# Kernel tuning notes

Hardware: AMD Instinct MI355X
Metric: run time of the kernel (lower is better)

The kernel has to match this reference:

```python
import jax, jax.numpy as jnp
import numpy as np

B, S, D_MODEL = 2, 2048, 4096
N_HEADS, N_KV, HEAD_DIM = 32, 8, 128
N_GROUPS = N_HEADS // N_KV
QKV_DIM = (N_HEADS + 2 * N_KV) * HEAD_DIM


def _rope_tables(seq_len, head_dim, base=10000.0):
    inv_freq = 1.0 / (base ** (np.arange(0, head_dim, 2, dtype=np.float32) / head_dim))
    t = np.arange(seq_len, dtype=np.float32)
    freqs = np.outer(t, inv_freq)                      # [S, D/2]
    emb = np.concatenate([freqs, freqs], axis=-1)      # [S, D]
    return jnp.asarray(np.cos(emb)), jnp.asarray(np.sin(emb))


def setup_inputs() -> dict:
    key = jax.random.key(0)
    k1, k2, k3 = jax.random.split(key, 3)
    cos, sin = _rope_tables(S, HEAD_DIM)
    return {
        "hidden_states": jax.random.normal(k1, (B, S, D_MODEL), dtype=jnp.float32),
        "cos": cos,
        "sin": sin,
        "W_qkv": jax.random.normal(k2, (D_MODEL, QKV_DIM), dtype=jnp.float32) * (D_MODEL ** -0.5),
        "W_out": jax.random.normal(k3, (D_MODEL, D_MODEL), dtype=jnp.float32) * (D_MODEL ** -0.5),
    }


def _rotate_half(x):
    x1, x2 = jnp.split(x, 2, axis=-1)
    return jnp.concatenate([-x2, x1], axis=-1)


def _apply_rope(x, cos, sin):
    # x: [b, h, s, d]; cos/sin: [s, d]
    c = cos[None, None, :, :]
    s = sin[None, None, :, :]
    return x * c + _rotate_half(x) * s


def reference(hidden_states, cos, sin, W_qkv, W_out):
    b, s, _ = hidden_states.shape
    qkv = jnp.einsum("bsm,mq->bsq", hidden_states, W_qkv)
    q_end = N_HEADS * HEAD_DIM
    kv_sz = N_KV * HEAD_DIM
    q = qkv[..., :q_end].reshape(b, s, N_HEADS, HEAD_DIM).transpose(0, 2, 1, 3)
    k = qkv[..., q_end:q_end + kv_sz].reshape(b, s, N_KV, HEAD_DIM).transpose(0, 2, 1, 3)
    v = qkv[..., q_end + kv_sz:].reshape(b, s, N_KV, HEAD_DIM).transpose(0, 2, 1, 3)

    q = _apply_rope(q, cos, sin)          # [b, H, s, d]
    k = _apply_rope(k, cos, sin)          # [b, KV, s, d] (equiv. to repeat->rope->stride slice)

    # GQA without materializing repeated KV: group query heads per KV head.
    qg = q.reshape(b, N_KV, N_GROUPS, s, HEAD_DIM)
    scale = HEAD_DIM ** -0.5
    scores = jnp.einsum("bkgqd,bkpd->bkgqp", qg, k) * scale  # [b, KV, G, s, s]
    causal = jnp.tril(jnp.ones((s, s), dtype=bool))
    scores = jnp.where(causal, scores, jnp.finfo(scores.dtype).min)
    probs = jax.nn.softmax(scores, axis=-1)
    out = jnp.einsum("bkgqp,bkpd->bkgqd", probs, v)           # [b, KV, G, s, d]
    out = out.reshape(b, N_HEADS, s, HEAD_DIM).transpose(0, 2, 1, 3).reshape(b, s, D_MODEL)
    return jnp.einsum("bsm,mn->bsn", out, W_out)
```

## Files before the change

### kernel.cpp

```cpp
#include <hip/hip_runtime.h>


typedef __bf16 bf16;
typedef bf16 bf16x8 __attribute__((ext_vector_type(8)));
typedef bf16 bf16x4 __attribute__((ext_vector_type(4)));
typedef float f32x4 __attribute__((ext_vector_type(4)));
typedef unsigned int u32;
typedef u32 u32x4 __attribute__((ext_vector_type(4)));

#define B_ 2
#define S_ 2048
#define DM 4096
#define NH 32
#define NKV 8
#define HD 128
#define QKV_DIM 6144

typedef __attribute__((address_space(3))) void lds_void;
typedef const __attribute__((address_space(1))) void glb_void;

__device__ __forceinline__ void gld_lds16(const bf16* g, bf16* l) {
  __builtin_amdgcn_global_load_lds((glb_void*)g, (lds_void*)l, 16, 0, 0);
}

__device__ __forceinline__ u32 bf16bits(float x) {
  union { bf16 h; unsigned short s; } u;
  u.h = (bf16)x;
  return (u32)u.s;
}

__global__ __launch_bounds__(256) void cast_f32_bf16(const float* __restrict__ src,
                                                     bf16* __restrict__ dst, int n) {
  int i = (blockIdx.x * 256 + threadIdx.x) * 4;
  float4 v = *(const float4*)(src + i);
  bf16x4 o;
  o[0] = (bf16)v.x; o[1] = (bf16)v.y; o[2] = (bf16)v.z; o[3] = (bf16)v.w;
  *(bf16x4*)(dst + i) = o;
}

__global__ __launch_bounds__(256) void transpose_cast_w(const float* __restrict__ W,
                                                        bf16* __restrict__ Wt,
                                                        int K, int N) {
  __shared__ float tile[64][65];
  const int n0 = blockIdx.x * 64, k0 = blockIdx.y * 64;
  const int t = threadIdx.x, j = t & 63, i0 = t >> 6;
  for (int p = 0; p < 16; ++p) {
    int i = i0 + p * 4;
    tile[i][j] = W[(size_t)(k0 + i) * N + n0 + j];
  }
  __syncthreads();
  for (int p = 0; p < 16; ++p) {
    int n = i0 + p * 4;
    Wt[(size_t)(n0 + n) * K + k0 + j] = (bf16)tile[j][n];
  }
}

__global__ __launch_bounds__(256) void transpose_v(const bf16* __restrict__ qkv,
                                                   bf16* __restrict__ v_t) {
  __shared__ bf16 tile[64][65];
  const int s0 = blockIdx.x * 64;
  const int d0 = blockIdx.y * 64;
  const int bk = blockIdx.z;
  const int b = bk >> 3, kv = bk & 7;
  const int t = threadIdx.x, j = t & 63, i0 = t >> 6;
  const bf16* src = qkv + (size_t)b * S_ * QKV_DIM + 5120 + kv * HD;
  for (int p = 0; p < 16; ++p) {
    int i = i0 + p * 4;
    tile[i][j] = src[(size_t)(s0 + i) * QKV_DIM + d0 + j];
  }
  __syncthreads();
  bf16* dst = v_t + ((size_t)bk * HD + d0) * S_ + s0;
  for (int p = 0; p < 16; ++p) {
    int dd = i0 + p * 4;
    dst[(size_t)dd * S_ + j] = tile[j][dd];
  }
}

__global__ __launch_bounds__(128) void rope_kernel(const bf16* __restrict__ qkv,
                                                   const float* __restrict__ cosT,
                                                   const float* __restrict__ sinT,
                                                   bf16* __restrict__ q_r,
                                                   bf16* __restrict__ k_r) {
  const int bs = blockIdx.x;
  const int b = bs >> 11, s = bs & 2047;
  const int d = threadIdx.x;
  const float cv = cosT[s * HD + d];
  const float sv = sinT[s * HD + d];
  const bf16* row = qkv + (size_t)bs * QKV_DIM;
  const float scale = 0.08838834764831845f;
  for (int h = 0; h < NH; ++h) {
    float x = (float)row[h * HD + d];
    float xr = (d < 64) ? -(float)row[h * HD + d + 64] : (float)row[h * HD + d - 64];
    q_r[(((size_t)(b * NH + h)) * S_ + s) * HD + d] = (bf16)((x * cv + xr * sv) * scale);
  }
  for (int kv = 0; kv < NKV; ++kv) {
    float x = (float)row[DM + kv * HD + d];
    float xr = (d < 64) ? -(float)row[DM + kv * HD + d + 64] : (float)row[DM + kv * HD + d - 64];
    k_r[(((size_t)(b * NKV + kv)) * S_ + s) * HD + d] = (bf16)(x * cv + xr * sv);
  }
}

template <bool OUT_BF16>
__global__ __launch_bounds__(256) void gemm_bt(const bf16* __restrict__ A,
                                               const bf16* __restrict__ Bt,
                                               void* __restrict__ Cout,
                                               int M, int N, int K) {
  __shared__ bf16 As[128 * 32];
  __shared__ bf16 Bs[128 * 32];
  const int m0 = blockIdx.y * 128, n0 = blockIdx.x * 128;
  const int t = threadIdx.x;
  const int lane = t & 63, w = t >> 6;
  const int wm = (w >> 1) * 64, wn = (w & 1) * 64;
  const int quad = lane >> 4, c = lane & 15;

  f32x4 acc[4][4] = {};

  const int s0i = t;
  const int r0 = s0i >> 2, c0 = (s0i & 3) * 8;
  const int s1i = 256 + t;
  const int r1 = s1i >> 2, c1 = (s1i & 3) * 8;
  const bf16* Ap0 = A + (size_t)(m0 + r0) * K + c0;
  const bf16* Ap1 = A + (size_t)(m0 + r1) * K + c1;
  const bf16* Bp0 = Bt + (size_t)(n0 + r0) * K + c0;
  const bf16* Bp1 = Bt + (size_t)(n0 + r1) * K + c1;
  bf16* Asl0 = As + (size_t)(w * 64) * 8;
  bf16* Asl1 = As + (size_t)(256 + w * 64) * 8;
  bf16* Bsl0 = Bs + (size_t)(w * 64) * 8;
  bf16* Bsl1 = Bs + (size_t)(256 + w * 64) * 8;

  for (int k0 = 0; k0 < K; k0 += 32) {
    gld_lds16(Ap0 + k0, Asl0);
    gld_lds16(Ap1 + k0, Asl1);
    gld_lds16(Bp0 + k0, Bsl0);
    gld_lds16(Bp1 + k0, Bsl1);
    __syncthreads();

    bf16x8 af[4], bfr[4];
#pragma unroll
    for (int i = 0; i < 4; ++i)
      af[i] = *(const bf16x8*)(As + (wm + i * 16 + c) * 32 + quad * 8);
#pragma unroll
    for (int j = 0; j < 4; ++j)
      bfr[j] = *(const bf16x8*)(Bs + (wn + j * 16 + c) * 32 + quad * 8);
#pragma unroll
    for (int i = 0; i < 4; ++i)
#pragma unroll
      for (int j = 0; j < 4; ++j)
        acc[i][j] = __builtin_amdgcn_mfma_f32_16x16x32_bf16(af[i], bfr[j], acc[i][j], 0, 0, 0);
    __syncthreads();
  }

#pragma unroll
  for (int i = 0; i < 4; ++i)
#pragma unroll
    for (int j = 0; j < 4; ++j) {
      const int row = m0 + wm + i * 16 + quad * 4;
      const int col = n0 + wn + j * 16 + c;
      if constexpr (OUT_BF16) {
        bf16* Cp = (bf16*)Cout;
#pragma unroll
        for (int r = 0; r < 4; ++r) Cp[(size_t)(row + r) * N + col] = (bf16)acc[i][j][r];
      } else {
        float* Cp = (float*)Cout;
#pragma unroll
        for (int r = 0; r < 4; ++r) Cp[(size_t)(row + r) * N + col] = acc[i][j][r];
      }
    }
}

#define SKS 136
#define SVS 40
__global__ __launch_bounds__(256) void attn_kernel(const bf16* __restrict__ q_r,
                                                   const bf16* __restrict__ k_r,
                                                   const bf16* __restrict__ v_t,
                                                   bf16* __restrict__ attn_out) {
  __shared__ bf16 Ks[32 * SKS];
  __shared__ bf16 Vs[128 * SVS];

  const int bh = blockIdx.x;
  const int b = bh >> 5, h = bh & 31;
  const int kv = h >> 2;
  const int q0 = blockIdx.y * 64;
  const int t = threadIdx.x, w = t >> 6, lane = t & 63;
  const int quad = lane >> 4, c = lane & 15;
  const int myq = q0 + w * 16 + c;

  const bf16* qrow = q_r + ((size_t)(b * NH + h) * S_ + myq) * HD;
  bf16x8 qf[4];
#pragma unroll
  for (int kk = 0; kk < 4; ++kk) qf[kk] = *(const bf16x8*)(qrow + quad * 8 + kk * 32);

  float m_i = -1e30f, l_i = 0.f;
  f32x4 o_acc[8];
#pragma unroll
  for (int n = 0; n < 8; ++n) o_acc[n] = (f32x4){0.f, 0.f, 0.f, 0.f};

  const bf16* kb_ptr = k_r + (size_t)(b * NKV + kv) * S_ * HD;
  const bf16* vb_ptr = v_t + (size_t)(b * NKV + kv) * HD * S_;

  const int nch = (q0 + 64) >> 5;
  const int ks_key = t >> 3, ks_doff = (t & 7) * 16;
  const int vs_d = t >> 1, vs_koff = (t & 1) * 16;
  const int src0 = c + 32 * (quad & 1);
  const int src1 = src0 + 16;
  const bool hiTile = (quad & 2) != 0;

  for (int ch = 0; ch < nch; ++ch) {
    const int kb = ch * 32;
    __syncthreads();
    {
      const bf16* kp = kb_ptr + (size_t)(kb + ks_key) * HD + ks_doff;
      bf16x8 kv0 = *(const bf16x8*)(kp);
      bf16x8 kv1 = *(const bf16x8*)(kp + 8);
      const bf16* vp = vb_ptr + (size_t)vs_d * S_ + kb + vs_koff;
      bf16x8 vv0 = *(const bf16x8*)(vp);
      bf16x8 vv1 = *(const bf16x8*)(vp + 8);
      *(bf16x8*)(Ks + ks_key * SKS + ks_doff) = kv0;
      *(bf16x8*)(Ks + ks_key * SKS + ks_doff + 8) = kv1;
      *(bf16x8*)(Vs + vs_d * SVS + vs_koff) = vv0;
      *(bf16x8*)(Vs + vs_d * SVS + vs_koff + 8) = vv1;
    }
    __syncthreads();

    if (kb <= q0 + w * 16 + 15) {
      f32x4 st0 = (f32x4){0.f, 0.f, 0.f, 0.f};
      f32x4 st1 = (f32x4){0.f, 0.f, 0.f, 0.f};
#pragma unroll
      for (int kk = 0; kk < 4; ++kk) {
        bf16x8 kf0 = *(const bf16x8*)(Ks + c * SKS + quad * 8 + kk * 32);
        bf16x8 kf1 = *(const bf16x8*)(Ks + (16 + c) * SKS + quad * 8 + kk * 32);
        st0 = __builtin_amdgcn_mfma_f32_16x16x32_bf16(kf0, qf[kk], st0, 0, 0, 0);
        st1 = __builtin_amdgcn_mfma_f32_16x16x32_bf16(kf1, qf[kk], st1, 0, 0, 0);
      }

      float v0[4], v1[4];
      const bool needMask = (kb + 31 > q0 + w * 16);
#pragma unroll
      for (int r = 0; r < 4; ++r) { v0[r] = st0[r]; v1[r] = st1[r]; }
      if (needMask) {
        const int key0 = kb + quad * 4;
#pragma unroll
        for (int r = 0; r < 4; ++r) {
          if (key0 + r > myq) v0[r] = -1e30f;
          if (key0 + 16 + r > myq) v1[r] = -1e30f;
        }
      }

      float mloc = fmaxf(fmaxf(fmaxf(v0[0], v0[1]), fmaxf(v0[2], v0[3])),
                         fmaxf(fmaxf(v1[0], v1[1]), fmaxf(v1[2], v1[3])));
      mloc = fmaxf(mloc, __shfl_xor(mloc, 16, 64));
      mloc = fmaxf(mloc, __shfl_xor(mloc, 32, 64));
      const float mnew = fmaxf(m_i, mloc);
      float e0[4], e1[4];
      float sum = 0.f;
#pragma unroll
      for (int r = 0; r < 4; ++r) {
        e0[r] = __expf(v0[r] - mnew);
        e1[r] = __expf(v1[r] - mnew);
        sum += e0[r] + e1[r];
      }
      sum += __shfl_xor(sum, 16, 64);
      sum += __shfl_xor(sum, 32, 64);
      const float alpha = __expf(m_i - mnew);
      m_i = mnew;
      l_i = l_i * alpha + sum;

      u32 pk[4];
#pragma unroll
      for (int r = 0; r < 4; ++r) pk[r] = bf16bits(e0[r]) | (bf16bits(e1[r]) << 16);
      u32 a0[4], a1[4];
#pragma unroll
      for (int r = 0; r < 4; ++r) {
        a0[r] = (u32)__shfl((int)pk[r], src0, 64);
        a1[r] = (u32)__shfl((int)pk[r], src1, 64);
      }
      u32 w0, w1, w2, w3;
      if (hiTile) {
        w0 = (a0[0] >> 16) | (a0[1] & 0xffff0000u);
        w1 = (a0[2] >> 16) | (a0[3] & 0xffff0000u);
        w2 = (a1[0] >> 16) | (a1[1] & 0xffff0000u);
        w3 = (a1[2] >> 16) | (a1[3] & 0xffff0000u);
      } else {
        w0 = (a0[0] & 0xffffu) | (a0[1] << 16);
        w1 = (a0[2] & 0xffffu) | (a0[3] << 16);
        w2 = (a1[0] & 0xffffu) | (a1[1] << 16);
        w3 = (a1[2] & 0xffffu) | (a1[3] << 16);
      }
      bf16x8 pf = __builtin_bit_cast(bf16x8, (u32x4){w0, w1, w2, w3});

      float alpha_o[4];
#pragma unroll
      for (int r = 0; r < 4; ++r) alpha_o[r] = __shfl(alpha, quad * 4 + r, 64);

#pragma unroll
      for (int n = 0; n < 8; ++n) {
#pragma unroll
        for (int r = 0; r < 4; ++r) o_acc[n][r] *= alpha_o[r];
      }
#pragma unroll
      for (int n = 0; n < 8; ++n) {
        bf16x8 vf = *(const bf16x8*)(Vs + (n * 16 + c) * SVS + quad * 8);
        o_acc[n] = __builtin_amdgcn_mfma_f32_16x16x32_bf16(pf, vf, o_acc[n], 0, 0, 0);
      }
    }
  }

  float l_o[4];
#pragma unroll
  for (int r = 0; r < 4; ++r) l_o[r] = __shfl(l_i, quad * 4 + r, 64);
#pragma unroll
  for (int n = 0; n < 8; ++n)
#pragma unroll
    for (int r = 0; r < 4; ++r) {
      const int row = q0 + w * 16 + quad * 4 + r;
      const float ov = o_acc[n][r] / l_o[r];
      attn_out[((size_t)b * S_ + row) * DM + h * HD + n * 16 + c] = (bf16)ov;
    }
}

extern "C" void kernel_launch(void* const* d_in, const int* in_sizes, int n_in,
                              void* d_out, int out_size, void* d_ws, size_t ws_size,
                              hipStream_t stream) {
  const float* hidden = (const float*)d_in[0];
  const float* cosT = (const float*)d_in[1];
  const float* sinT = (const float*)d_in[2];
  const float* Wqkv = (const float*)d_in[3];
  const float* Wout = (const float*)d_in[4];
  float* out = (float*)d_out;
  char* ws = (char*)d_ws;

  bf16* WqkvT = (bf16*)(ws + 0);
  bf16* q_r = (bf16*)(ws + 0);
  bf16* k_r = (bf16*)(ws + 33554432);
  bf16* WoutT = (bf16*)(ws + 50331648);
  bf16* h_bf = (bf16*)(ws + 83886080);
  bf16* attn_out = (bf16*)(ws + 83886080);
  bf16* v_t = (bf16*)(ws + 117440512);
  bf16* qkv = (bf16*)d_out;

  cast_f32_bf16<<<dim3(16384), dim3(256), 0, stream>>>(hidden, h_bf, B_ * S_ * DM);
  transpose_cast_w<<<dim3(QKV_DIM / 64, DM / 64), dim3(256), 0, stream>>>(Wqkv, WqkvT, DM, QKV_DIM);
  transpose_cast_w<<<dim3(DM / 64, DM / 64), dim3(256), 0, stream>>>(Wout, WoutT, DM, DM);
  gemm_bt<true><<<dim3(QKV_DIM / 128, (B_ * S_) / 128), dim3(256), 0, stream>>>(
      h_bf, WqkvT, (void*)qkv, B_ * S_, QKV_DIM, DM);
  rope_kernel<<<dim3(B_ * S_), dim3(128), 0, stream>>>(qkv, cosT, sinT, q_r, k_r);
  transpose_v<<<dim3(S_ / 64, HD / 64, B_ * NKV), dim3(256), 0, stream>>>(qkv, v_t);
  attn_kernel<<<dim3(B_ * NH, S_ / 64), dim3(256), 0, stream>>>(q_r, k_r, v_t, attn_out);
  gemm_bt<false><<<dim3(DM / 128, (B_ * S_) / 128), dim3(256), 0, stream>>>(
      attn_out, WoutT, (void*)out, B_ * S_, DM, DM);
}
```

Baseline: 933.1 us.

## Replace GEMM with 256x256 tiled, double-buffered, swizzled-LDS pipelined kernel

Replaces the simple 128x128 single-buffered GEMM with a 256x256 tile kernel using 512 threads, 128KB dynamic LDS double-buffered across K tiles, XOR-swizzled LDS layout, XCD-aware workgroup remapping, and manual vmcnt/barrier scheduling with s_setprio around MFMA bursts. It aims to hide global load latency and raise MFMA utilization for both projection GEMMs. The larger tile and 128KB LDS limit occupancy and rely on the hand-tuned waitcnt counts being correct.

```diff
diff --git a/kernel.cpp b/kernel.cpp
--- a/kernel.cpp
+++ b/kernel.cpp
@@ -100,70 +100,136 @@
   }
 }
 
+#define BAR() __builtin_amdgcn_s_barrier()
+#define LGKM0() asm volatile("s_waitcnt lgkmcnt(0)" ::: "memory")
+#define VM6() asm volatile("s_waitcnt vmcnt(6)" ::: "memory")
+#define VM0() asm volatile("s_waitcnt vmcnt(0)" ::: "memory")
+#define VMNONE() do {} while (0)
+#define PRIO1() __builtin_amdgcn_s_setprio(1)
+#define PRIO0() __builtin_amdgcn_s_setprio(0)
+
+#define MFMA16(MH)                                                                   \
+  do {                                                                               \
+    _Pragma("unroll") for (int mm = 0; mm < 4; ++mm) {                               \
+      _Pragma("unroll") for (int nn = 0; nn < 4; ++nn) {                             \
+        acc[(MH)*4 + mm][nn] = __builtin_amdgcn_mfma_f32_16x16x32_bf16(              \
+            af[mm], bfr[nn], acc[(MH)*4 + mm][nn], 0, 0, 0);                         \
+      }                                                                              \
+    }                                                                                \
+  } while (0)
+
+#define TILE4(T, P, VMEND)                                                           \
+  do {                                                                               \
+    ldA(P, 0, 0); ldB(P, 0);                                                         \
+    stage_idx(4 * (T) + 7);                                                          \
+    BAR(); LGKM0();                                                                  \
+    PRIO1(); MFMA16(0); PRIO0(); BAR();                                              \
+    ldA(P, 0, 1);                                                                    \
+    stage_idx(4 * (T) + 8);                                                          \
+    BAR(); LGKM0();                                                                  \
+    PRIO1(); MFMA16(1); PRIO0(); BAR();                                              \
+    ldA(P, 1, 0); ldB(P, 1);                                                         \
+    stage_idx(4 * (T) + 9);                                                          \
+    BAR(); LGKM0();                                                                  \
+    PRIO1(); MFMA16(0); PRIO0(); BAR();                                              \
+    ldA(P, 1, 1);                                                                    \
+    stage_idx(4 * (T) + 10);                                                         \
+    BAR(); LGKM0();                                                                  \
+    PRIO1(); MFMA16(1); PRIO0();                                                     \
+    VMEND; BAR();                                                                    \
+  } while (0)
+
 template <bool OUT_BF16>
-__global__ __launch_bounds__(256) void gemm_bt(const bf16* __restrict__ A,
-                                               const bf16* __restrict__ Bt,
-                                               void* __restrict__ Cout,
-                                               int M, int N, int K) {
-  __shared__ bf16 As[128 * 32];
-  __shared__ bf16 Bs[128 * 32];
-  const int m0 = blockIdx.y * 128, n0 = blockIdx.x * 128;
+__global__ __launch_bounds__(512, 2) void gemm256_bt(const bf16* __restrict__ A,
+                                                     const bf16* __restrict__ Bt,
+                                                     void* __restrict__ Cout,
+                                                     int M, int N, int K) {
+  extern __shared__ char lds[];
+  const int NT = K >> 6;
+
+  const int nwg = gridDim.x;
+  const int cpx = nwg >> 3;
+  const int wg = (blockIdx.x & 7) * cpx + (blockIdx.x >> 3);
+  const int nbx = N >> 8;
+  const int bx = wg % nbx, by = wg / nbx;
+  const int m0 = by * 256, n0 = bx * 256;
+
   const int t = threadIdx.x;
-  const int lane = t & 63, w = t >> 6;
-  const int wm = (w >> 1) * 64, wn = (w & 1) * 64;
+  const int w = t >> 6, lane = t & 63;
+  const int wr = w >> 2, wc = w & 3;
   const int quad = lane >> 4, c = lane & 15;
 
-  f32x4 acc[4][4] = {};
-
-  const int s0i = t;
-  const int r0 = s0i >> 2, c0 = (s0i & 3) * 8;
-  const int s1i = 256 + t;
-  const int r1 = s1i >> 2, c1 = (s1i & 3) * 8;
-  const bf16* Ap0 = A + (size_t)(m0 + r0) * K + c0;
-  const bf16* Ap1 = A + (size_t)(m0 + r1) * K + c1;
-  const bf16* Bp0 = Bt + (size_t)(n0 + r0) * K + c0;
-  const bf16* Bp1 = Bt + (size_t)(n0 + r1) * K + c1;
-  bf16* Asl0 = As + (size_t)(w * 64) * 8;
-  bf16* Asl1 = As + (size_t)(256 + w * 64) * 8;
-  bf16* Bsl0 = Bs + (size_t)(w * 64) * 8;
-  bf16* Bsl1 = Bs + (size_t)(256 + w * 64) * 8;
-
-  for (int k0 = 0; k0 < K; k0 += 32) {
-    gld_lds16(Ap0 + k0, Asl0);
-    gld_lds16(Ap1 + k0, Asl1);
-    gld_lds16(Bp0 + k0, Bsl0);
-    gld_lds16(Bp1 + k0, Bsl1);
-    __syncthreads();
-
-    bf16x8 af[4], bfr[4];
-#pragma unroll
-    for (int i = 0; i < 4; ++i)
-      af[i] = *(const bf16x8*)(As + (wm + i * 16 + c) * 32 + quad * 8);
-#pragma unroll
-    for (int j = 0; j < 4; ++j)
-      bfr[j] = *(const bf16x8*)(Bs + (wn + j * 16 + c) * 32 + quad * 8);
-#pragma unroll
-    for (int i = 0; i < 4; ++i)
-#pragma unroll
-      for (int j = 0; j < 4; ++j)
-        acc[i][j] = __builtin_amdgcn_mfma_f32_16x16x32_bf16(af[i], bfr[j], acc[i][j], 0, 0, 0);
-    __syncthreads();
-  }
-
-#pragma unroll
-  for (int i = 0; i < 4; ++i)
-#pragma unroll
-    for (int j = 0; j < 4; ++j) {
-      const int row = m0 + wm + i * 16 + quad * 4;
-      const int col = n0 + wn + j * 16 + c;
+  const int aOff = (((wr * 128 + c) * 64 + quad * 16) ^ ((c & 8) << 2));
+  const int bOff = (((wc * 64 + c) * 64 + quad * 16) ^ ((c & 8) << 2)) + 32768;
+
+  const int srow = w * 32 + (lane >> 2);
+  const int scol = (((lane & 3) ^ ((lane >> 4) & 2)) << 3);
+  const bf16* Abase = A + (size_t)(m0 + srow) * K + scol;
+  const bf16* Bbase = Bt + (size_t)(n0 + srow) * K + scol;
+  const size_t rs16 = (size_t)16 * K;
+
+  auto stage_idx = [&](int H) {
+    if (H >= 4 * NT) return;
+    const int tS = H >> 2, jS = H & 3;
+    const int kh = jS >> 1;
+    const int kbase = tS * 64 + kh * 32;
+    const int regionOff = ((tS & 1) << 16) + ((jS & 1) << 15) + (kh << 14) + (w << 11);
+    const bf16* g = ((jS & 1) ? Bbase : Abase) + kbase;
+    char* l = lds + regionOff;
+    gld_lds16(g, (bf16*)l);
+    gld_lds16(g + rs16, (bf16*)(l + 1024));
+  };
+
+  bf16x8 af[4], bfr[4];
+  auto ldA = [&](int P, int s, int mh) {
+    const char* base = lds + P * 65536 + s * 16384 + mh * 4096 + aOff;
+    af[0] = *(const bf16x8*)(base);
+    af[1] = *(const bf16x8*)(base + 1024);
+    af[2] = *(const bf16x8*)(base + 2048);
+    af[3] = *(const bf16x8*)(base + 3072);
+  };
+  auto ldB = [&](int P, int s) {
+    const char* base = lds + P * 65536 + s * 16384 + bOff;
+    bfr[0] = *(const bf16x8*)(base);
+    bfr[1] = *(const bf16x8*)(base + 1024);
+    bfr[2] = *(const bf16x8*)(base + 2048);
+    bfr[3] = *(const bf16x8*)(base + 3072);
+  };
+
+  f32x4 acc[8][4];
+#pragma unroll
+  for (int i = 0; i < 8; ++i)
+#pragma unroll
+    for (int j = 0; j < 4; ++j) acc[i][j] = (f32x4){0.f, 0.f, 0.f, 0.f};
+
+#pragma unroll
+  for (int hh = 0; hh < 7; ++hh) stage_idx(hh);
+  VM6();
+  BAR();
+
+  for (int tt = 0; tt < NT - 2; tt += 2) {
+    TILE4(tt, 0, VM6());
+    TILE4(tt + 1, 1, VM6());
+  }
+  TILE4(NT - 2, 0, VM0());
+  TILE4(NT - 1, 1, VMNONE());
+
+  const int crow = m0 + wr * 128 + quad * 4;
+  const int ccol = n0 + wc * 64 + c;
+#pragma unroll
+  for (int mf = 0; mf < 8; ++mf)
+#pragma unroll
+    for (int nn = 0; nn < 4; ++nn) {
+      const int row = crow + mf * 16;
+      const int col = ccol + nn * 16;
       if constexpr (OUT_BF16) {
         bf16* Cp = (bf16*)Cout;
 #pragma unroll
-        for (int r = 0; r < 4; ++r) Cp[(size_t)(row + r) * N + col] = (bf16)acc[i][j][r];
+        for (int r = 0; r < 4; ++r) Cp[(size_t)(row + r) * N + col] = (bf16)acc[mf][nn][r];
       } else {
         float* Cp = (float*)Cout;
 #pragma unroll
-        for (int r = 0; r < 4; ++r) Cp[(size_t)(row + r) * N + col] = acc[i][j][r];
+        for (int r = 0; r < 4; ++r) Cp[(size_t)(row + r) * N + col] = acc[mf][nn][r];
       }
     }
 }
@@ -338,14 +404,23 @@
   bf16* v_t = (bf16*)(ws + 117440512);
   bf16* qkv = (bf16*)d_out;
 
+  static bool attr_set = false;
+  if (!attr_set) {
+    hipFuncSetAttribute(reinterpret_cast<const void*>(&gemm256_bt<true>),
+                        hipFuncAttributeMaxDynamicSharedMemorySize, 131072);
+    hipFuncSetAttribute(reinterpret_cast<const void*>(&gemm256_bt<false>),
+                        hipFuncAttributeMaxDynamicSharedMemorySize, 131072);
+    attr_set = true;
+  }
+
   cast_f32_bf16<<<dim3(16384), dim3(256), 0, stream>>>(hidden, h_bf, B_ * S_ * DM);
   transpose_cast_w<<<dim3(QKV_DIM / 64, DM / 64), dim3(256), 0, stream>>>(Wqkv, WqkvT, DM, QKV_DIM);
   transpose_cast_w<<<dim3(DM / 64, DM / 64), dim3(256), 0, stream>>>(Wout, WoutT, DM, DM);
-  gemm_bt<true><<<dim3(QKV_DIM / 128, (B_ * S_) / 128), dim3(256), 0, stream>>>(
+  gemm256_bt<true><<<dim3((QKV_DIM / 256) * ((B_ * S_) / 256)), dim3(512), 131072, stream>>>(
       h_bf, WqkvT, (void*)qkv, B_ * S_, QKV_DIM, DM);
   rope_kernel<<<dim3(B_ * S_), dim3(128), 0, stream>>>(qkv, cosT, sinT, q_r, k_r);
   transpose_v<<<dim3(S_ / 64, HD / 64, B_ * NKV), dim3(256), 0, stream>>>(qkv, v_t);
   attn_kernel<<<dim3(B_ * NH, S_ / 64), dim3(256), 0, stream>>>(q_r, k_r, v_t, attn_out);
-  gemm_bt<false><<<dim3(DM / 128, (B_ * S_) / 128), dim3(256), 0, stream>>>(
+  gemm256_bt<false><<<dim3((DM / 256) * ((B_ * S_) / 256)), dim3(512), 131072, stream>>>(
       attn_out, WoutT, (void*)out, B_ * S_, DM, DM);
 }
```

Result: faster. 807.2 us (-13.5%).
